# Kernel optimization log

Hardware: AMD Instinct MI355X
Metric: run time of the kernel (lower is better)

## Reference

```python
import jax, jax.numpy as jnp
import numpy as np

NUM_SRC = 100000   # in_features
NUM_DST = 100000   # out_features
NNZ = 3_200_000
BATCH = 16


def setup_inputs() -> dict:
    key = jax.random.key(0)
    k_x, k_v, k_b, k_r, k_c = jax.random.split(key, 5)
    x = jax.random.normal(k_x, (BATCH, NUM_SRC), dtype=jnp.float32)
    values = jax.random.normal(k_v, (NNZ,), dtype=jnp.float32)
    bias = jax.random.normal(k_b, (NUM_DST,), dtype=jnp.float32)
    row = jax.random.randint(k_r, (NNZ,), 0, NUM_DST)   # dst index
    col = jax.random.randint(k_c, (NNZ,), 0, NUM_SRC)   # src index
    indices = jnp.stack([row, col], axis=0).astype(jnp.int64)
    return {"x": x, "values": values, "bias": bias, "indices": indices}


def reference(x, values, bias, indices):
    """out[b, d] = sum_{e: row[e]==d} values[e] * x[b, col[e]] + bias[d].

    Equivalent to torch.sparse.mm(coo(indices, values, (DST, SRC)), x.T).T + bias,
    with the effective weight being the raw value parameter (identity
    _get_effective_weight, recomputed each call).
    """
    row, col = indices[0], indices[1]
    # per-edge contributions: (nnz, B)
    contrib = values[:, None] * x.T[col]
    out = jax.ops.segment_sum(contrib, row, num_segments=NUM_DST)  # (DST, B)
    return out.T + bias  # (B, DST)
```

## Files before the change

kernel.cpp:

```cpp
#include <hip/hip_runtime.h>

#define NUM_SRC 100000
#define NUM_DST 100000
#define NNZ     3200000
#define BATCH   16

#define BIN_SHIFT 7
#define ROWS_PER_BIN 128
#define NBIN 782
#define BIN_CAP 4544
#define TILE 4096
#define NTILE ((NNZ + TILE - 1) / TILE)
#define PTHR 512
#define EPT (TILE / PTHR)
#define EPT_B ((BIN_CAP + 511) / 512)

__device__ __forceinline__ float lo16(unsigned u) { return __uint_as_float(u << 16); }
__device__ __forceinline__ float hi16(unsigned u) { return __uint_as_float(u & 0xFFFF0000u); }

__global__ void k_transpose_cast(const float* __restrict__ x,
                                 ushort* __restrict__ xT16,
                                 unsigned* __restrict__ gcur) {
    int s = blockIdx.x * blockDim.x + threadIdx.x;
    if (s < NBIN) gcur[s] = 0u;
    if (s >= NUM_SRC) return;
    unsigned u[BATCH];
#pragma unroll
    for (int b = 0; b < BATCH; ++b) {
        unsigned bits = __float_as_uint(x[(long)b * NUM_SRC + s]);
        u[b] = (bits + 0x7FFFu + ((bits >> 16) & 1u)) >> 16;
    }
    uint4 w0, w1;
    w0.x = u[0]  | (u[1]  << 16);
    w0.y = u[2]  | (u[3]  << 16);
    w0.z = u[4]  | (u[5]  << 16);
    w0.w = u[6]  | (u[7]  << 16);
    w1.x = u[8]  | (u[9]  << 16);
    w1.y = u[10] | (u[11] << 16);
    w1.z = u[12] | (u[13] << 16);
    w1.w = u[14] | (u[15] << 16);
    uint4* dst = reinterpret_cast<uint4*>(xT16 + (long)s * BATCH);
    dst[0] = w0; dst[1] = w1;
}

__global__ __launch_bounds__(PTHR) void k_partition(const float* __restrict__ values,
                                                    const int*  __restrict__ row,
                                                    const int*  __restrict__ col,
                                                    unsigned*   __restrict__ gcur,
                                                    uint2*      __restrict__ packed) {
    __shared__ uint2    srt[TILE];
    __shared__ unsigned hist[NBIN];
    __shared__ unsigned offs[NBIN];
    __shared__ unsigned gb[NBIN];
    __shared__ unsigned sum8[99];
    int t = threadIdx.x;
    long e0 = (long)blockIdx.x * TILE;
    int n = (int)min((long)TILE, (long)NNZ - e0);

    for (int i = t; i < NBIN; i += PTHR) hist[i] = 0;
    __syncthreads();

    int rr[EPT]; int cc[EPT]; float vv[EPT];
    bool valid = (t * EPT) < n;
    if (valid) {
        const int4*   r4 = reinterpret_cast<const int4*>(row + e0) + 2 * t;
        const int4*   c4 = reinterpret_cast<const int4*>(col + e0) + 2 * t;
        const float4* v4 = reinterpret_cast<const float4*>(values + e0) + 2 * t;
        int4 ra = r4[0], rb = r4[1];
        int4 ca = c4[0], cb = c4[1];
        float4 va = v4[0], vb = v4[1];
        rr[0]=ra.x; rr[1]=ra.y; rr[2]=ra.z; rr[3]=ra.w;
        rr[4]=rb.x; rr[5]=rb.y; rr[6]=rb.z; rr[7]=rb.w;
        cc[0]=ca.x; cc[1]=ca.y; cc[2]=ca.z; cc[3]=ca.w;
        cc[4]=cb.x; cc[5]=cb.y; cc[6]=cb.z; cc[7]=cb.w;
        vv[0]=va.x; vv[1]=va.y; vv[2]=va.z; vv[3]=va.w;
        vv[4]=vb.x; vv[5]=vb.y; vv[6]=vb.z; vv[7]=vb.w;
    } else {
#pragma unroll
        for (int k = 0; k < EPT; ++k) rr[k] = -1;
    }
#pragma unroll
    for (int k = 0; k < EPT; ++k)
        if (rr[k] >= 0) atomicAdd(&hist[(unsigned)rr[k] >> BIN_SHIFT], 1u);
    __syncthreads();

    if (t < 98) {
        unsigned s = 0;
        int b0 = t * 8, b1 = min(b0 + 8, NBIN);
        for (int b = b0; b < b1; ++b) { offs[b] = s; s += hist[b]; }
        sum8[t] = s;
    }
    __syncthreads();
    if (t < 64) {
        unsigned c0 = (2*t   < 98) ? sum8[2*t]   : 0u;
        unsigned c1 = (2*t+1 < 98) ? sum8[2*t+1] : 0u;
        unsigned pair = c0 + c1;
        unsigned incl = pair;
#pragma unroll
        for (int off = 1; off < 64; off <<= 1) {
            unsigned up = (unsigned)__shfl_up((int)incl, off, 64);
            if (t >= off) incl += up;
        }
        unsigned excl = incl - pair;
        if (2*t   < 98) sum8[2*t]   = excl;
        if (2*t+1 < 98) sum8[2*t+1] = excl + c0;
    }
    __syncthreads();
    for (int b = t; b < NBIN; b += PTHR) offs[b] += sum8[b >> 3];
    __syncthreads();

    for (int b = t; b < NBIN; b += PTHR) {
        unsigned len = hist[b];
        gb[b] = len ? atomicAdd(&gcur[b], len) : 0u;
    }

    unsigned pos[EPT];
#pragma unroll
    for (int k = 0; k < EPT; ++k)
        if (rr[k] >= 0)
            pos[k] = atomicAdd(&offs[(unsigned)rr[k] >> BIN_SHIFT], 1u);
#pragma unroll
    for (int k = 0; k < EPT; ++k) {
        if (rr[k] >= 0) {
            uint2 rec;
            rec.x = ((unsigned)(rr[k] & (ROWS_PER_BIN - 1)) << 17) | (unsigned)cc[k];
            rec.y = __float_as_uint(vv[k]);
            srt[pos[k]] = rec;
        }
    }
    __syncthreads();

    for (int b = t >> 3; b < NBIN; b += 64) {
        unsigned len = hist[b];
        if (!len) continue;
        unsigned start = offs[b] - len;
        unsigned gbase = gb[b];
        uint2* dst = packed + (long)b * BIN_CAP + gbase;
        for (unsigned j = t & 7; j < len; j += 8)
            if (gbase + j < BIN_CAP)
                dst[j] = srt[start + j];
    }
}

__global__ __launch_bounds__(512) void k_bucket_sorted(const uint2* __restrict__ packed,
                                                       const unsigned* __restrict__ gcur,
                                                       const ushort* __restrict__ xT16,
                                                       const float* __restrict__ bias,
                                                       float* __restrict__ out) {
    __shared__ uint2    srt[BIN_CAP];
    __shared__ float    accf[ROWS_PER_BIN * 17];
    __shared__ unsigned cnt[ROWS_PER_BIN];
    __shared__ unsigned starts[ROWS_PER_BIN + 1];
    __shared__ unsigned offs[ROWS_PER_BIN];
    int t = threadIdx.x;
    int bin = blockIdx.x;
    int n = min((int)gcur[bin], BIN_CAP);
    const uint2* base = packed + (long)bin * BIN_CAP;

    for (int i = t; i < ROWS_PER_BIN; i += 512) cnt[i] = 0;
    __syncthreads();

    uint2 rec[EPT_B];
#pragma unroll
    for (int k = 0; k < EPT_B; ++k) {
        int i = t + k * 512;
        rec[k].x = 0xFFFFFFFFu;
        if (i < n) rec[k] = base[i];
    }
#pragma unroll
    for (int k = 0; k < EPT_B; ++k)
        if (rec[k].x != 0xFFFFFFFFu) atomicAdd(&cnt[rec[k].x >> 17], 1u);
    __syncthreads();

    if (t < 64) {
        unsigned c0 = cnt[2 * t], c1 = cnt[2 * t + 1];
        unsigned pair = c0 + c1;
        unsigned incl = pair;
#pragma unroll
        for (int off = 1; off < 64; off <<= 1) {
            unsigned up = (unsigned)__shfl_up((int)incl, off, 64);
            if (t >= off) incl += up;
        }
        unsigned excl = incl - pair;
        starts[2 * t]     = excl;
        starts[2 * t + 1] = excl + c0;
        if (t == 63) starts[ROWS_PER_BIN] = incl;
    }
    __syncthreads();
    for (int i = t; i < ROWS_PER_BIN; i += 512) offs[i] = starts[i];
    __syncthreads();

    unsigned pos[EPT_B];
#pragma unroll
    for (int k = 0; k < EPT_B; ++k)
        if (rec[k].x != 0xFFFFFFFFu)
            pos[k] = atomicAdd(&offs[rec[k].x >> 17], 1u);
#pragma unroll
    for (int k = 0; k < EPT_B; ++k)
        if (rec[k].x != 0xFFFFFFFFu)
            srt[pos[k]] = rec[k];
    __syncthreads();

    int g  = t >> 4;
    int ro = (t >> 2) & 3;
    int bs = t & 3;
    const ushort* xbs = xT16 + bs * 4;

#pragma unroll
    for (int q = 0; q < 4; ++q) {
        int r  = g + 32 * q;
        int j0 = (int)starts[r];
        int e  = (int)starts[r + 1];
        int j  = j0 + ro;
        int nit = (e - j + 3) >> 2;
        float ac0 = 0.f, ac1 = 0.f, ac2 = 0.f, ac3 = 0.f;

        bool a0 = j     < e;
        bool a1 = j + 4 < e;
        bool a2 = j + 8 < e;
        uint2 r0 = srt[a0 ? j     : 0];
        uint2 r1 = srt[a1 ? j + 4 : 0];
        uint2 r2 = srt[a2 ? j + 8 : 0];
        float v0 = a0 ? __uint_as_float(r0.y) : 0.f;
        float v1 = a1 ? __uint_as_float(r1.y) : 0.f;
        float v2 = a2 ? __uint_as_float(r2.y) : 0.f;
        uint2 x0 = *reinterpret_cast<const uint2*>(xbs + (long)(r0.x & 0x1FFFFu) * BATCH);
        uint2 x1 = *reinterpret_cast<const uint2*>(xbs + (long)(r1.x & 0x1FFFFu) * BATCH);
        uint2 x2 = *reinterpret_cast<const uint2*>(xbs + (long)(r2.x & 0x1FFFFu) * BATCH);
        int jn = j + 12;

        for (int it = 0; it < nit; ++it) {
            ac0 = fmaf(v0, lo16(x0.x), ac0);
            ac1 = fmaf(v0, hi16(x0.x), ac1);
            ac2 = fmaf(v0, lo16(x0.y), ac2);
            ac3 = fmaf(v0, hi16(x0.y), ac3);
            v0 = v1; x0 = x1;
            v1 = v2; x1 = x2;
            bool a = jn < e;
            uint2 rc = srt[a ? jn : 0];
            v2 = a ? __uint_as_float(rc.y) : 0.f;
            x2 = *reinterpret_cast<const uint2*>(xbs + (long)(rc.x & 0x1FFFFu) * BATCH);
            jn += 4;
        }

        ac0 += __shfl_xor(ac0, 4); ac0 += __shfl_xor(ac0, 8);
        ac1 += __shfl_xor(ac1, 4); ac1 += __shfl_xor(ac1, 8);
        ac2 += __shfl_xor(ac2, 4); ac2 += __shfl_xor(ac2, 8);
        ac3 += __shfl_xor(ac3, 4); ac3 += __shfl_xor(ac3, 8);
        if (ro == 0) {
            float* arow = accf + r * 17 + bs * 4;
            arow[0] = ac0; arow[1] = ac1; arow[2] = ac2; arow[3] = ac3;
        }
    }
    __syncthreads();

    int dbase = bin * ROWS_PER_BIN;
    for (int i = t; i < ROWS_PER_BIN * BATCH; i += 512) {
        int bb = i >> 7;
        int r  = i & 127;
        int d  = dbase + r;
        if (d < NUM_DST)
            out[(long)bb * NUM_DST + d] = accf[r * 17 + bb] + bias[d];
    }
}

extern "C" void kernel_launch(void* const* d_in, const int* in_sizes, int n_in,
                              void* d_out, int out_size, void* d_ws, size_t ws_size,
                              hipStream_t stream) {
    const float* x      = (const float*)d_in[0];
    const float* values = (const float*)d_in[1];
    const float* bias   = (const float*)d_in[2];
    const int*   idx    = (const int*)  d_in[3];
    const int* row = idx;
    const int* col = idx + NNZ;
    float* out = (float*)d_out;

    ushort*   xT16   = (ushort*)d_ws;
    uint2*    packed = (uint2*)((char*)d_ws + (size_t)NUM_SRC * BATCH * sizeof(ushort));
    unsigned* gcur   = (unsigned*)((char*)packed + (size_t)NBIN * BIN_CAP * sizeof(uint2));

    {
        int blocks = (NUM_SRC + 255) / 256;
        k_transpose_cast<<<blocks, 256, 0, stream>>>(x, xT16, gcur);
    }
    k_partition<<<NTILE, PTHR, 0, stream>>>(values, row, col, gcur, packed);
    k_bucket_sorted<<<NBIN, 512, 0, stream>>>(packed, gcur, xT16, bias, out);
}
```

Measured before the change: 147.8 us.

## Replace global atomic bin scatter with per-tile sorted dump and offset table

The partition kernel now writes each tile's locally bin-sorted records contiguously, using coalesced 16-byte stores, plus a per-tile table of bin offsets. This replaces the global atomic bin cursors and the scattered per-bin copies. A new kernel transposes the offset table so that each bin block can prefix-sum the per-tile segment lengths and gather its records from all 782 tiles. The gather is a serial per-thread loop over small segments with uncoalesced reads, and it is done twice (count pass and scatter pass), which may cost more than the global atomics it replaces. It also adds an extra kernel launch.

```diff
diff --git a/kernel.cpp b/kernel.cpp
--- a/kernel.cpp
+++ b/kernel.cpp
@@ -13,16 +13,13 @@
 #define NTILE ((NNZ + TILE - 1) / TILE)
 #define PTHR 512
 #define EPT (TILE / PTHR)
-#define EPT_B ((BIN_CAP + 511) / 512)
 
 __device__ __forceinline__ float lo16(unsigned u) { return __uint_as_float(u << 16); }
 __device__ __forceinline__ float hi16(unsigned u) { return __uint_as_float(u & 0xFFFF0000u); }
 
 __global__ void k_transpose_cast(const float* __restrict__ x,
-                                 ushort* __restrict__ xT16,
-                                 unsigned* __restrict__ gcur) {
+                                 ushort* __restrict__ xT16) {
     int s = blockIdx.x * blockDim.x + threadIdx.x;
-    if (s < NBIN) gcur[s] = 0u;
     if (s >= NUM_SRC) return;
     unsigned u[BATCH];
 #pragma unroll
@@ -46,12 +43,11 @@
 __global__ __launch_bounds__(PTHR) void k_partition(const float* __restrict__ values,
                                                     const int*  __restrict__ row,
                                                     const int*  __restrict__ col,
-                                                    unsigned*   __restrict__ gcur,
-                                                    uint2*      __restrict__ packed) {
+                                                    uint2*      __restrict__ pk,
+                                                    unsigned*   __restrict__ ST) {
     __shared__ uint2    srt[TILE];
     __shared__ unsigned hist[NBIN];
     __shared__ unsigned offs[NBIN];
-    __shared__ unsigned gb[NBIN];
     __shared__ unsigned sum8[99];
     int t = threadIdx.x;
     long e0 = (long)blockIdx.x * TILE;
@@ -109,10 +105,10 @@
     for (int b = t; b < NBIN; b += PTHR) offs[b] += sum8[b >> 3];
     __syncthreads();
 
-    for (int b = t; b < NBIN; b += PTHR) {
-        unsigned len = hist[b];
-        gb[b] = len ? atomicAdd(&gcur[b], len) : 0u;
-    }
+    unsigned* strow = ST + (long)blockIdx.x * (NBIN + 1);
+    for (int b = t; b < NBIN; b += PTHR) strow[b] = offs[b];
+    if (t == 0) strow[NBIN] = (unsigned)n;
+    __syncthreads();
 
     unsigned pos[EPT];
 #pragma unroll
@@ -130,20 +126,32 @@
     }
     __syncthreads();
 
-    for (int b = t >> 3; b < NBIN; b += 64) {
-        unsigned len = hist[b];
-        if (!len) continue;
-        unsigned start = offs[b] - len;
-        unsigned gbase = gb[b];
-        uint2* dst = packed + (long)b * BIN_CAP + gbase;
-        for (unsigned j = t & 7; j < len; j += 8)
-            if (gbase + j < BIN_CAP)
-                dst[j] = srt[start + j];
-    }
-}
-
-__global__ __launch_bounds__(512) void k_bucket_sorted(const uint2* __restrict__ packed,
-                                                       const unsigned* __restrict__ gcur,
+    const uint4* s4 = reinterpret_cast<const uint4*>(srt);
+    uint4* d4 = reinterpret_cast<uint4*>(pk + (size_t)blockIdx.x * TILE);
+#pragma unroll
+    for (int i = t; i < TILE / 2; i += PTHR) d4[i] = s4[i];
+}
+
+__global__ void k_transpose_table(const unsigned* __restrict__ ST,
+                                  unsigned* __restrict__ STT) {
+    __shared__ unsigned tile[32][33];
+    int x = blockIdx.x * 32 + threadIdx.x;
+    for (int dy = threadIdx.y; dy < 32; dy += 8) {
+        int y = blockIdx.y * 32 + dy;
+        tile[dy][threadIdx.x] = (y < NTILE && x < NBIN + 1)
+            ? ST[(long)y * (NBIN + 1) + x] : 0u;
+    }
+    __syncthreads();
+    int xx = blockIdx.y * 32 + threadIdx.x;
+    for (int dy = threadIdx.y; dy < 32; dy += 8) {
+        int yy = blockIdx.x * 32 + dy;
+        if (yy < NBIN + 1 && xx < NTILE)
+            STT[(long)yy * NTILE + xx] = tile[threadIdx.x][dy];
+    }
+}
+
+__global__ __launch_bounds__(512) void k_bucket_sorted(const uint2* __restrict__ pk,
+                                                       const unsigned* __restrict__ STT,
                                                        const ushort* __restrict__ xT16,
                                                        const float* __restrict__ bias,
                                                        float* __restrict__ out) {
@@ -152,24 +160,60 @@
     __shared__ unsigned cnt[ROWS_PER_BIN];
     __shared__ unsigned starts[ROWS_PER_BIN + 1];
     __shared__ unsigned offs[ROWS_PER_BIN];
+    __shared__ unsigned s0t[NTILE];
+    __shared__ unsigned pft[NTILE + 1];
+    __shared__ unsigned csum[99];
     int t = threadIdx.x;
-    int bin = blockIdx.x;
-    int n = min((int)gcur[bin], BIN_CAP);
-    const uint2* base = packed + (long)bin * BIN_CAP;
-
+    int b = blockIdx.x;
+
+    const unsigned* r0 = STT + (long)b * NTILE;
+    const unsigned* r1 = STT + (long)(b + 1) * NTILE;
+#pragma unroll
+    for (int k = 0; k < 2; ++k) {
+        int i = t + k * 512;
+        if (i < NTILE) { unsigned a = r0[i]; s0t[i] = a; pft[i] = r1[i] - a; }
+    }
     for (int i = t; i < ROWS_PER_BIN; i += 512) cnt[i] = 0;
     __syncthreads();
 
-    uint2 rec[EPT_B];
-#pragma unroll
-    for (int k = 0; k < EPT_B; ++k) {
+    if (t < 98) {
+        unsigned s = 0;
+        int i0 = t * 8, i1 = min(i0 + 8, NTILE);
+        for (int i = i0; i < i1; ++i) { unsigned v = pft[i]; pft[i] = s; s += v; }
+        csum[t] = s;
+    }
+    __syncthreads();
+    if (t < 64) {
+        unsigned c0 = (2*t   < 98) ? csum[2*t]   : 0u;
+        unsigned c1 = (2*t+1 < 98) ? csum[2*t+1] : 0u;
+        unsigned pair = c0 + c1;
+        unsigned incl = pair;
+#pragma unroll
+        for (int off = 1; off < 64; off <<= 1) {
+            unsigned up = (unsigned)__shfl_up((int)incl, off, 64);
+            if (t >= off) incl += up;
+        }
+        unsigned excl = incl - pair;
+        if (2*t   < 98) csum[2*t]   = excl;
+        if (2*t+1 < 98) csum[2*t+1] = excl + c0;
+        if (t == 48) pft[NTILE] = incl;
+    }
+    __syncthreads();
+    for (int i = t; i < NTILE; i += 512) pft[i] += csum[i >> 3];
+    __syncthreads();
+
+#pragma unroll
+    for (int k = 0; k < 2; ++k) {
         int i = t + k * 512;
-        rec[k].x = 0xFFFFFFFFu;
-        if (i < n) rec[k] = base[i];
-    }
-#pragma unroll
-    for (int k = 0; k < EPT_B; ++k)
-        if (rec[k].x != 0xFFFFFFFFu) atomicAdd(&cnt[rec[k].x >> 17], 1u);
+        if (i < NTILE) {
+            unsigned src = (unsigned)i * TILE + s0t[i];
+            unsigned len = pft[i + 1] - pft[i];
+            for (unsigned j = 0; j < len; ++j) {
+                uint2 rc = pk[src + j];
+                atomicAdd(&cnt[rc.x >> 17], 1u);
+            }
+        }
+    }
     __syncthreads();
 
     if (t < 64) {
@@ -190,15 +234,19 @@
     for (int i = t; i < ROWS_PER_BIN; i += 512) offs[i] = starts[i];
     __syncthreads();
 
-    unsigned pos[EPT_B];
-#pragma unroll
-    for (int k = 0; k < EPT_B; ++k)
-        if (rec[k].x != 0xFFFFFFFFu)
-            pos[k] = atomicAdd(&offs[rec[k].x >> 17], 1u);
-#pragma unroll
-    for (int k = 0; k < EPT_B; ++k)
-        if (rec[k].x != 0xFFFFFFFFu)
-            srt[pos[k]] = rec[k];
+#pragma unroll
+    for (int k = 0; k < 2; ++k) {
+        int i = t + k * 512;
+        if (i < NTILE) {
+            unsigned src = (unsigned)i * TILE + s0t[i];
+            unsigned len = pft[i + 1] - pft[i];
+            for (unsigned j = 0; j < len; ++j) {
+                uint2 rc = pk[src + j];
+                unsigned pos = atomicAdd(&offs[rc.x >> 17], 1u);
+                if (pos < BIN_CAP) srt[pos] = rc;
+            }
+        }
+    }
     __syncthreads();
 
     int g  = t >> 4;
@@ -209,8 +257,8 @@
 #pragma unroll
     for (int q = 0; q < 4; ++q) {
         int r  = g + 32 * q;
-        int j0 = (int)starts[r];
-        int e  = (int)starts[r + 1];
+        int j0 = min((int)starts[r], BIN_CAP);
+        int e  = min((int)starts[r + 1], BIN_CAP);
         int j  = j0 + ro;
         int nit = (e - j + 3) >> 2;
         float ac0 = 0.f, ac1 = 0.f, ac2 = 0.f, ac3 = 0.f;
@@ -218,15 +266,15 @@
         bool a0 = j     < e;
         bool a1 = j + 4 < e;
         bool a2 = j + 8 < e;
-        uint2 r0 = srt[a0 ? j     : 0];
-        uint2 r1 = srt[a1 ? j + 4 : 0];
-        uint2 r2 = srt[a2 ? j + 8 : 0];
-        float v0 = a0 ? __uint_as_float(r0.y) : 0.f;
-        float v1 = a1 ? __uint_as_float(r1.y) : 0.f;
-        float v2 = a2 ? __uint_as_float(r2.y) : 0.f;
-        uint2 x0 = *reinterpret_cast<const uint2*>(xbs + (long)(r0.x & 0x1FFFFu) * BATCH);
-        uint2 x1 = *reinterpret_cast<const uint2*>(xbs + (long)(r1.x & 0x1FFFFu) * BATCH);
-        uint2 x2 = *reinterpret_cast<const uint2*>(xbs + (long)(r2.x & 0x1FFFFu) * BATCH);
+        uint2 r0_ = srt[a0 ? j     : 0];
+        uint2 r1_ = srt[a1 ? j + 4 : 0];
+        uint2 r2_ = srt[a2 ? j + 8 : 0];
+        float v0 = a0 ? __uint_as_float(r0_.y) : 0.f;
+        float v1 = a1 ? __uint_as_float(r1_.y) : 0.f;
+        float v2 = a2 ? __uint_as_float(r2_.y) : 0.f;
+        uint2 x0 = *reinterpret_cast<const uint2*>(xbs + (long)(r0_.x & 0x1FFFFu) * BATCH);
+        uint2 x1 = *reinterpret_cast<const uint2*>(xbs + (long)(r1_.x & 0x1FFFFu) * BATCH);
+        uint2 x2 = *reinterpret_cast<const uint2*>(xbs + (long)(r2_.x & 0x1FFFFu) * BATCH);
         int jn = j + 12;
 
         for (int it = 0; it < nit; ++it) {
@@ -254,7 +302,7 @@
     }
     __syncthreads();
 
-    int dbase = bin * ROWS_PER_BIN;
+    int dbase = b * ROWS_PER_BIN;
     for (int i = t; i < ROWS_PER_BIN * BATCH; i += 512) {
         int bb = i >> 7;
         int r  = i & 127;
@@ -275,14 +323,21 @@
     const int* col = idx + NNZ;
     float* out = (float*)d_out;
 
-    ushort*   xT16   = (ushort*)d_ws;
-    uint2*    packed = (uint2*)((char*)d_ws + (size_t)NUM_SRC * BATCH * sizeof(ushort));
-    unsigned* gcur   = (unsigned*)((char*)packed + (size_t)NBIN * BIN_CAP * sizeof(uint2));
+    char* w = (char*)d_ws;
+    ushort*   xT16 = (ushort*)w;                        w += (size_t)NUM_SRC * BATCH * sizeof(ushort);
+    uint2*    pk   = (uint2*)w;                         w += (size_t)NTILE * TILE * sizeof(uint2);
+    unsigned* ST   = (unsigned*)w;                      w += (size_t)NTILE * (NBIN + 1) * sizeof(unsigned);
+    unsigned* STT  = (unsigned*)w;
 
     {
         int blocks = (NUM_SRC + 255) / 256;
-        k_transpose_cast<<<blocks, 256, 0, stream>>>(x, xT16, gcur);
-    }
-    k_partition<<<NTILE, PTHR, 0, stream>>>(values, row, col, gcur, packed);
-    k_bucket_sorted<<<NBIN, 512, 0, stream>>>(packed, gcur, xT16, bias, out);
-}
+        k_transpose_cast<<<blocks, 256, 0, stream>>>(x, xT16);
+    }
+    k_partition<<<NTILE, PTHR, 0, stream>>>(values, row, col, pk, ST);
+    {
+        dim3 grid((NBIN + 32) / 32, (NTILE + 31) / 32);
+        dim3 blk(32, 8);
+        k_transpose_table<<<grid, blk, 0, stream>>>(ST, STT);
+    }
+    k_bucket_sorted<<<NBIN, 512, 0, stream>>>(pk, STT, xT16, bias, out);
+}
```

New measurement: 191.6 us. +29.7%, slower.
